# Kernel tuning notes

Measured on AMD Instinct MI355X. Metric: run time of the kernel, lower is better.

Reference implementation:

```python
import jax, jax.numpy as jnp
import numpy as np

KH = KW = 3
STRIDE = 1
ITERATIONS = 2
EPS = 1e-7


def _squash(s):
    # squash along last axis (capsule dim)
    sn = jnp.sum(s * s, axis=-1, keepdims=True)
    return (sn / (1.0 + sn)) * s / jnp.sqrt(sn + EPS)


def setup_inputs() -> dict:
    key = jax.random.key(0)
    k1, k2 = jax.random.split(key)
    x = jax.random.normal(k1, (4, 14, 14, 32, 8), dtype=jnp.float32)
    # W: [1,1,1,filters_out, caps_per_patch=3*3*32, dims_out=16, dims_in=8], stddev=0.1 init
    W = 0.1 * jax.random.normal(k2, (1, 1, 1, 32, 288, 16, 8), dtype=jnp.float32)
    return {"x": x, "W": W}


def reference(x, W):
    B, H, Wd, Fin, Din = x.shape
    Ho = (H - KH) // STRIDE + 1
    Wo = (Wd - KW) // STRIDE + 1
    # Patch extraction, channel order (kh, kw, Fin) to match tf.image.extract_patches
    patches = jnp.stack(
        [x[:, i:i + Ho * STRIDE:STRIDE, j:j + Wo * STRIDE:STRIDE]
         for i in range(KH) for j in range(KW)],
        axis=3,
    )  # [B,Ho,Wo,KH*KW,Fin,Din]
    patches = patches.reshape(B, Ho, Wo, KH * KW * Fin, Din)  # [B,Ho,Wo,C,Di]

    Wm = W[0, 0, 0]  # [F, C, Do, Di]
    F, C, Do, _ = Wm.shape
    # predictions[b,h,w,f,c,o] = sum_i W[f,c,o,i] * patches[b,h,w,c,i]
    preds = jnp.einsum('fcoi,bhwci->bhwfco', Wm, patches)

    logits = jnp.zeros((B, Ho, Wo, F, C), dtype=preds.dtype)
    outputs = jnp.zeros((B, Ho, Wo, F, Do), dtype=preds.dtype)
    for _ in range(ITERATIONS):
        # agreement = predictions^T @ outputs over the dims_out axis
        agreement = jnp.einsum('bhwfco,bhwfo->bhwfc', preds, outputs)
        logits = logits + agreement
        # NOTE: original code softmaxes over axis=3 (the filters_out axis)
        cc = jax.nn.softmax(logits, axis=3)  # [B,Ho,Wo,F,C]
        centroids = jnp.sum(cc[..., None] * preds, axis=4)  # [B,Ho,Wo,F,Do]
        outputs = _squash(centroids)
    return outputs
```

## Files before the change

### kernel.cpp

```cpp
#include <hip/hip_runtime.h>

#define NB   4
#define H_IN 14
#define W_IN 14
#define FIN  32
#define DI   8
#define F    32
#define C    288
#define DO   16
#define HO   12
#define WO   12
#define NPOS (NB*HO*WO)
#define EPS  1e-7f

#define CH   16
#define CC   (C/CH)
#define GP   8
#define GRID (CH*(NPOS/GP))

#define KTOT (C*DI)

#define W2H_BYTES  ((size_t)F*C*DO*DI*2)
#define WH_BYTES   ((size_t)F*C*DO*DI*2)
#define PH_BYTES   ((size_t)NPOS*KTOT*2)
#define PART_BYTES ((size_t)CH*NPOS*F*DO*4)
#define OUT1_BYTES ((size_t)NPOS*F*DO*4)

#define CVT_W2H 576
#define CVT_WH  576
#define CVT_PH  648
#define CVT_GRID (CVT_W2H + CVT_WH + CVT_PH)

typedef _Float16 h2 __attribute__((ext_vector_type(2)));
typedef _Float16 h8v __attribute__((ext_vector_type(8)));
typedef float    f4v __attribute__((ext_vector_type(4)));

__device__ __forceinline__ unsigned int pack2(float a, float b) {
    h2 v; v.x = (_Float16)a; v.y = (_Float16)b;
    return __builtin_bit_cast(unsigned int, v);
}

__device__ __forceinline__ float dot8h(const uint4 w, const uint4 v, float acc) {
#if __has_builtin(__builtin_amdgcn_fdot2)
    acc = __builtin_amdgcn_fdot2(__builtin_bit_cast(h2, w.x), __builtin_bit_cast(h2, v.x), acc, false);
    acc = __builtin_amdgcn_fdot2(__builtin_bit_cast(h2, w.y), __builtin_bit_cast(h2, v.y), acc, false);
    acc = __builtin_amdgcn_fdot2(__builtin_bit_cast(h2, w.z), __builtin_bit_cast(h2, v.z), acc, false);
    acc = __builtin_amdgcn_fdot2(__builtin_bit_cast(h2, w.w), __builtin_bit_cast(h2, v.w), acc, false);
#else
    const h2 w0 = __builtin_bit_cast(h2, w.x), v0 = __builtin_bit_cast(h2, v.x);
    const h2 w1 = __builtin_bit_cast(h2, w.y), v1 = __builtin_bit_cast(h2, v.y);
    const h2 w2 = __builtin_bit_cast(h2, w.z), v2 = __builtin_bit_cast(h2, v.z);
    const h2 w3 = __builtin_bit_cast(h2, w.w), v3 = __builtin_bit_cast(h2, v.w);
    acc += (float)w0.x*(float)v0.x + (float)w0.y*(float)v0.y
         + (float)w1.x*(float)v1.x + (float)w1.y*(float)v1.y
         + (float)w2.x*(float)v2.x + (float)w2.y*(float)v2.y
         + (float)w3.x*(float)v3.x + (float)w3.y*(float)v3.y;
#endif
    return acc;
}

__device__ __forceinline__ int xbase_of(int pos) {
    const int b = pos/(HO*WO), rem = pos%(HO*WO), ho = rem/WO, wo = rem%WO;
    return ((b*H_IN + ho)*W_IN + wo)*FIN*DI;
}

__device__ __forceinline__ int coff_of(int c) {
    const int slab = c >> 5, fin = c & 31;
    const int kh = slab/3, kw = slab%3;
    return (kh*W_IN + kw)*FIN*DI + fin*DI;
}

__global__ __launch_bounds__(256) void kernConv(const float* __restrict__ Wt,
                                                const float* __restrict__ x,
                                                unsigned short* __restrict__ W2h,
                                                unsigned short* __restrict__ Wh,
                                                unsigned short* __restrict__ Ph) {
    const int b = blockIdx.x;
    if (b < CVT_W2H) {
        const int idx = b*256 + threadIdx.x;
        const int f = idx & 31, o = (idx >> 5) & 15, c = idx >> 9;
        const float* src = Wt + ((size_t)(f*C + c)*DO + o)*DI;
        const float4 a = *(const float4*)src;
        const float4 bb = *(const float4*)(src + 4);
        uint4 r;
        r.x = pack2(a.x, a.y);   r.y = pack2(a.z, a.w);
        r.z = pack2(bb.x, bb.y); r.w = pack2(bb.z, bb.w);
        ((uint4*)W2h)[idx] = r;
    } else if (b < CVT_W2H + CVT_WH) {
        const int idx = (b - CVT_W2H)*256 + threadIdx.x;
        const float* src = Wt + (size_t)idx*8;
        const float4 a = *(const float4*)src;
        const float4 bb = *(const float4*)(src + 4);
        uint4 r;
        r.x = pack2(a.x, a.y);   r.y = pack2(a.z, a.w);
        r.z = pack2(bb.x, bb.y); r.w = pack2(bb.z, bb.w);
        ((uint4*)Wh)[idx] = r;
    } else {
        const int pc = (b - CVT_W2H - CVT_WH)*256 + threadIdx.x;
        const int pos = pc / C, c = pc % C;
        const float* src = x + xbase_of(pos) + coff_of(c);
        const float4 a = *(const float4*)src;
        const float4 bb = *(const float4*)(src + 4);
        uint4 r;
        r.x = pack2(a.x, a.y);   r.y = pack2(a.z, a.w);
        r.z = pack2(bb.x, bb.y); r.w = pack2(bb.z, bb.w);
        ((uint4*)Ph)[pc] = r;
    }
}

__global__ __launch_bounds__(256) void kernM1(const unsigned short* __restrict__ Ph,
                                              const unsigned short* __restrict__ Wh,
                                              float* __restrict__ out1)
{
    const int lane = threadIdx.x & 63;
    const int wv   = threadIdx.x >> 6;
    const int f    = blockIdx.x & 31;
    const int pt   = (blockIdx.x >> 5)*4 + wv;
    const int pos0 = pt*16;
    const int n    = lane & 15, q = lane >> 4;

    const unsigned short* pa = Ph + (size_t)(pos0 + n)*KTOT + q*8;
    const unsigned short* pb = Wh + ((size_t)(f*C + q)*DO + n)*DI;

    f4v acc0 = {0.f,0.f,0.f,0.f}, acc1 = {0.f,0.f,0.f,0.f};
    #pragma unroll 4
    for (int s = 0; s < KTOT/32; s += 2) {
        const h8v a0 = *(const h8v*)(pa + (size_t)s*32);
        const h8v b0 = *(const h8v*)(pb + (size_t)s*4*DO*DI);
        const h8v a1 = *(const h8v*)(pa + (size_t)(s+1)*32);
        const h8v b1 = *(const h8v*)(pb + (size_t)(s+1)*4*DO*DI);
        acc0 = __builtin_amdgcn_mfma_f32_16x16x32_f16(a0, b0, acc0, 0, 0, 0);
        acc1 = __builtin_amdgcn_mfma_f32_16x16x32_f16(a1, b1, acc1, 0, 0, 0);
    }

    #pragma unroll
    for (int r = 0; r < 4; ++r) {
        const float v = (acc0[r] + acc1[r]) * (1.f/32.f);
        float sq = v*v;
        sq += __shfl_xor(sq, 1);
        sq += __shfl_xor(sq, 2);
        sq += __shfl_xor(sq, 4);
        sq += __shfl_xor(sq, 8);
        const float sc = (sq/(1.f + sq)) * rsqrtf(sq + EPS);
        out1[(size_t)(pos0 + q*4 + r)*512 + f*DO + n] = v * sc;
    }
}

__global__ __launch_bounds__(256) void kern2n(const unsigned short* __restrict__ Ph,
                                              const unsigned short* __restrict__ W2h,
                                              const float* __restrict__ out1,
                                              float* __restrict__ part2)
{
    __shared__ float red[2][4][GP][32];
    __shared__ float ccs[2][GP][32];

    const int tid = threadIdx.x;
    const int f  = tid & 31;
    const int og = tid >> 5;
    const int o0 = 2*og, o1 = o0 + 1;
    const int wv = tid >> 6;
    const int half = (tid >> 5) & 1;
    const int ch = blockIdx.x & (CH-1);
    const int pg = blockIdx.x >> 4;

    int poff[GP];
    #pragma unroll
    for (int p = 0; p < GP; ++p) poff[p] = (pg*GP + p)*KTOT;

    float u0[GP], u1[GP];
    #pragma unroll
    for (int p = 0; p < GP; ++p) {
        const float* up = out1 + (size_t)(pg*GP + p)*512 + f*DO;
        u0[p] = up[o0];
        u1[p] = up[o1];
    }

    const uint4* W2h4 = (const uint4*)W2h;
    const int c0 = ch*CC;

    float acc0[GP], acc1[GP];
    #pragma unroll
    for (int p = 0; p < GP; ++p) { acc0[p] = 0.f; acc1[p] = 0.f; }

    #pragma unroll 1
    for (int cl = 0; cl < CC; ++cl) {
        const int c = c0 + cl;
        const int buf = cl & 1;
        const uint4 w0 = W2h4[(size_t)(c*DO + o0)*F + f];
        const uint4 w1 = W2h4[(size_t)(c*DO + o1)*F + f];

        float pred0[GP], pred1[GP];
        #pragma unroll
        for (int p = 0; p < GP; ++p) {
            const uint4 xv = *(const uint4*)(Ph + poff[p] + c*DI);
            pred0[p] = dot8h(w0, xv, 0.f);
            pred1[p] = dot8h(w1, xv, 0.f);
        }

        #pragma unroll
        for (int p = 0; p < GP; ++p) {
            float ap = pred0[p]*u0[p] + pred1[p]*u1[p];
            ap += __shfl_xor(ap, 32);
            if (half == 0) red[buf][wv][p][f] = ap;
        }
        __syncthreads();

        {
            const int p2 = tid >> 5, f2 = tid & 31;
            const float agr = red[buf][0][p2][f2] + red[buf][1][p2][f2]
                            + red[buf][2][p2][f2] + red[buf][3][p2][f2];
            float m = agr;
            m = fmaxf(m, __shfl_xor(m, 1));
            m = fmaxf(m, __shfl_xor(m, 2));
            m = fmaxf(m, __shfl_xor(m, 4));
            m = fmaxf(m, __shfl_xor(m, 8));
            m = fmaxf(m, __shfl_xor(m, 16));
            const float e = __expf(agr - m);
            float s = e;
            s += __shfl_xor(s, 1);
            s += __shfl_xor(s, 2);
            s += __shfl_xor(s, 4);
            s += __shfl_xor(s, 8);
            s += __shfl_xor(s, 16);
            ccs[buf][p2][f2] = e / s;
        }
        __syncthreads();

        #pragma unroll
        for (int p = 0; p < GP; ++p) {
            const float cv = ccs[buf][p][f];
            acc0[p] += cv*pred0[p];
            acc1[p] += cv*pred1[p];
        }
    }

    #pragma unroll
    for (int p = 0; p < GP; ++p) {
        const size_t base = ((size_t)(ch*NPOS + pg*GP + p))*DO;
        part2[(base + o0)*F + f] = acc0[p];
        part2[(base + o1)*F + f] = acc1[p];
    }
}

__global__ __launch_bounds__(256) void kern3(const float* __restrict__ part2,
                                             float* __restrict__ out)
{
    const int tid = threadIdx.x;
    const int f = tid & 31, p = tid >> 5;
    const int pos = blockIdx.x*8 + p;

    float cent[DO];
    #pragma unroll
    for (int o = 0; o < DO; ++o) cent[o] = 0.f;
    #pragma unroll 1
    for (int k = 0; k < CH; ++k) {
        const float* s = part2 + (size_t)(k*NPOS + pos)*512 + f;
        #pragma unroll
        for (int o = 0; o < DO; ++o) cent[o] += s[o*F];
    }
    float sn = 0.f;
    #pragma unroll
    for (int o = 0; o < DO; ++o) sn += cent[o]*cent[o];
    const float sc = (sn/(1.f + sn)) * rsqrtf(sn + EPS);
    float* dst = out + ((size_t)pos*F + f)*DO;
    #pragma unroll
    for (int o = 0; o < DO; ++o) dst[o] = cent[o]*sc;
}

__device__ __forceinline__ float dot8(const float4* __restrict__ w,
                                      const float4 p0, const float4 p1) {
    float4 a = w[0], b = w[1];
    return a.x*p0.x + a.y*p0.y + a.z*p0.z + a.w*p0.w
         + b.x*p1.x + b.y*p1.y + b.z*p1.z + b.w*p1.w;
}

__global__ __launch_bounds__(256) void capsule_kernel_f32(
    const float* __restrict__ x, const float* __restrict__ Wt,
    float* __restrict__ out)
{
    __shared__ float patch[C*DI];
    __shared__ float cent[F*DO];
    __shared__ float out1[F*DO];
    __shared__ float agr[F*C];
    __shared__ float scale_s[F];

    const int tid = threadIdx.x;
    const int pos = blockIdx.x;
    const int b   = pos / (HO*WO);
    const int rem = pos % (HO*WO);
    const int ho  = rem / WO;
    const int wo  = rem % WO;

    #pragma unroll
    for (int slab = 0; slab < 9; ++slab) {
        const int kh = slab / 3, kw = slab % 3;
        const float* src = x + (((b*H_IN + ho + kh)*W_IN + (wo + kw))*FIN)*DI;
        patch[slab*256 + tid] = src[tid];
    }
    __syncthreads();

    const float4* pv = (const float4*)patch;

    {
        const int fo0 = tid, fo1 = tid + 256;
        const int f0 = fo0 >> 4, o0 = fo0 & 15;
        const int f1 = fo1 >> 4, o1 = fo1 & 15;
        float acc0 = 0.f, acc1 = 0.f;
        for (int c = 0; c < C; ++c) {
            const float4 p0 = pv[c*2], p1 = pv[c*2+1];
            acc0 += dot8((const float4*)(Wt + ((f0*C + c)*DO + o0)*DI), p0, p1);
            acc1 += dot8((const float4*)(Wt + ((f1*C + c)*DO + o1)*DI), p0, p1);
        }
        cent[fo0] = acc0 * (1.f/32.f);
        cent[fo1] = acc1 * (1.f/32.f);
    }
    __syncthreads();

    if (tid < F) {
        float sn = 0.f;
        #pragma unroll
        for (int o = 0; o < DO; ++o) { float v = cent[tid*DO + o]; sn += v*v; }
        const float sc = (sn/(1.f + sn)) * rsqrtf(sn + EPS);
        #pragma unroll
        for (int o = 0; o < DO; ++o) out1[tid*DO + o] = cent[tid*DO + o] * sc;
    }
    __syncthreads();

    #pragma unroll 1
    for (int r = 0; r < (F*C)/256; ++r) {
        const int pp = tid + 256*r;
        const int f = pp / C, c = pp % C;
        const float4* wrow = (const float4*)(Wt + (f*C + c)*DO*DI);
        const float4 p0 = pv[c*2], p1 = pv[c*2+1];
        float a = 0.f;
        #pragma unroll
        for (int o = 0; o < DO; ++o) a += dot8(wrow + o*2, p0, p1) * out1[f*DO + o];
        agr[pp] = a;
    }
    __syncthreads();

    for (int c = tid; c < C; c += 256) {
        float m = -1e30f;
        #pragma unroll
        for (int f = 0; f < F; ++f) m = fmaxf(m, agr[f*C + c]);
        float s = 0.f;
        #pragma unroll
        for (int f = 0; f < F; ++f) {
            const float e = __expf(agr[f*C + c] - m);
            agr[f*C + c] = e; s += e;
        }
        const float inv = 1.f / s;
        #pragma unroll
        for (int f = 0; f < F; ++f) agr[f*C + c] *= inv;
    }
    __syncthreads();

    {
        const int fo0 = tid, fo1 = tid + 256;
        const int f0 = fo0 >> 4, o0 = fo0 & 15;
        const int f1 = fo1 >> 4, o1 = fo1 & 15;
        float acc0 = 0.f, acc1 = 0.f;
        for (int c = 0; c < C; ++c) {
            const float4 p0 = pv[c*2], p1 = pv[c*2+1];
            acc0 += agr[f0*C + c] * dot8((const float4*)(Wt + ((f0*C + c)*DO + o0)*DI), p0, p1);
            acc1 += agr[f1*C + c] * dot8((const float4*)(Wt + ((f1*C + c)*DO + o1)*DI), p0, p1);
        }
        cent[fo0] = acc0;
        cent[fo1] = acc1;
    }
    __syncthreads();

    if (tid < F) {
        float sn = 0.f;
        #pragma unroll
        for (int o = 0; o < DO; ++o) { float v = cent[tid*DO + o]; sn += v*v; }
        scale_s[tid] = (sn/(1.f + sn)) * rsqrtf(sn + EPS);
    }
    __syncthreads();

    out[pos*(F*DO) + tid]       = cent[tid]       * scale_s[tid >> 4];
    out[pos*(F*DO) + tid + 256] = cent[tid + 256] * scale_s[(tid >> 4) + 16];
}

extern "C" void kernel_launch(void* const* d_in, const int* in_sizes, int n_in,
                              void* d_out, int out_size, void* d_ws, size_t ws_size,
                              hipStream_t stream) {
    const float* x  = (const float*)d_in[0];
    const float* Wt = (const float*)d_in[1];
    float* out = (float*)d_out;

    if (ws_size >= W2H_BYTES + WH_BYTES + PH_BYTES + PART_BYTES + OUT1_BYTES) {
        char* p = (char*)d_ws;
        unsigned short* W2h = (unsigned short*)p;            p += W2H_BYTES;
        unsigned short* Wh  = (unsigned short*)p;            p += WH_BYTES;
        unsigned short* Ph  = (unsigned short*)p;            p += PH_BYTES;
        float* part = (float*)p;                             p += PART_BYTES;
        float* out1 = (float*)p;

        kernConv<<<CVT_GRID, 256, 0, stream>>>(Wt, x, W2h, Wh, Ph);
        kernM1<<<(F/1)*9, 256, 0, stream>>>(Ph, Wh, out1);
        kern2n<<<GRID, 256, 0, stream>>>(Ph, W2h, out1, part);
        kern3<<<NPOS/8, 256, 0, stream>>>(part, out);
    } else {
        capsule_kernel_f32<<<NPOS, 256, 0, stream>>>(x, Wt, out);
    }
}
```

Measured before the change: 138.1 us.

## Stage patch tile in LDS shared across waves in kernM1; coalesce W2h reads

kernM1 now loads each 16-position patch tile once into padded shared memory. The four waves of a block each compute a different output filter from that shared tile, instead of each wave streaming the patches from global memory for its own position tile. The W2h conversion now reads the weights linearly and scatters its writes into the same [c][o][f] layout as before, swapping strided reads for strided writes. The shared tile uses about 74KB of LDS per block, which may limit occupancy and adds a block-wide barrier before the MFMA loop.

```diff
diff --git a/kernel.cpp b/kernel.cpp
--- a/kernel.cpp
+++ b/kernel.cpp
@@ -19,6 +19,7 @@
 #define GRID (CH*(NPOS/GP))
 
 #define KTOT (C*DI)
+#define KPAD 2312
 
 #define W2H_BYTES  ((size_t)F*C*DO*DI*2)
 #define WH_BYTES   ((size_t)F*C*DO*DI*2)
@@ -78,14 +79,16 @@
     const int b = blockIdx.x;
     if (b < CVT_W2H) {
         const int idx = b*256 + threadIdx.x;
-        const int f = idx & 31, o = (idx >> 5) & 15, c = idx >> 9;
-        const float* src = Wt + ((size_t)(f*C + c)*DO + o)*DI;
+        const float* src = Wt + (size_t)idx*8;
         const float4 a = *(const float4*)src;
         const float4 bb = *(const float4*)(src + 4);
         uint4 r;
         r.x = pack2(a.x, a.y);   r.y = pack2(a.z, a.w);
         r.z = pack2(bb.x, bb.y); r.w = pack2(bb.z, bb.w);
-        ((uint4*)W2h)[idx] = r;
+        const int o = idx & 15;
+        const int c = (idx >> 4) % C;
+        const int f = idx / (C*DO);
+        ((uint4*)W2h)[(size_t)(c*DO + o)*F + f] = r;
     } else if (b < CVT_W2H + CVT_WH) {
         const int idx = (b - CVT_W2H)*256 + threadIdx.x;
         const float* src = Wt + (size_t)idx*8;
@@ -112,22 +115,35 @@
                                               const unsigned short* __restrict__ Wh,
                                               float* __restrict__ out1)
 {
-    const int lane = threadIdx.x & 63;
-    const int wv   = threadIdx.x >> 6;
-    const int f    = blockIdx.x & 31;
-    const int pt   = (blockIdx.x >> 5)*4 + wv;
+    __shared__ unsigned short As[16][KPAD];
+
+    const int tid  = threadIdx.x;
+    const int lane = tid & 63;
+    const int wv   = tid >> 6;
+    const int pt   = blockIdx.x >> 3;
+    const int fg   = blockIdx.x & 7;
+    const int f    = wv*8 + fg;
     const int pos0 = pt*16;
     const int n    = lane & 15, q = lane >> 4;
 
-    const unsigned short* pa = Ph + (size_t)(pos0 + n)*KTOT + q*8;
+    #pragma unroll
+    for (int r = 0; r < 18; ++r) {
+        const int linear = r*256 + tid;
+        const int row = linear / 288, col8 = linear % 288;
+        const uint4 v = *(const uint4*)(Ph + (size_t)(pos0 + row)*KTOT + col8*8);
+        *(uint4*)&As[row][col8*8] = v;
+    }
+    __syncthreads();
+
+    const unsigned short* pa = &As[n][q*8];
     const unsigned short* pb = Wh + ((size_t)(f*C + q)*DO + n)*DI;
 
     f4v acc0 = {0.f,0.f,0.f,0.f}, acc1 = {0.f,0.f,0.f,0.f};
     #pragma unroll 4
     for (int s = 0; s < KTOT/32; s += 2) {
-        const h8v a0 = *(const h8v*)(pa + (size_t)s*32);
+        const h8v a0 = *(const h8v*)(pa + s*32);
         const h8v b0 = *(const h8v*)(pb + (size_t)s*4*DO*DI);
-        const h8v a1 = *(const h8v*)(pa + (size_t)(s+1)*32);
+        const h8v a1 = *(const h8v*)(pa + (s+1)*32);
         const h8v b1 = *(const h8v*)(pb + (size_t)(s+1)*4*DO*DI);
         acc0 = __builtin_amdgcn_mfma_f32_16x16x32_f16(a0, b0, acc0, 0, 0, 0);
         acc1 = __builtin_amdgcn_mfma_f32_16x16x32_f16(a1, b1, acc1, 0, 0, 0);
@@ -398,7 +414,7 @@
         float* out1 = (float*)p;
 
         kernConv<<<CVT_GRID, 256, 0, stream>>>(Wt, x, W2h, Wh, Ph);
-        kernM1<<<(F/1)*9, 256, 0, stream>>>(Ph, Wh, out1);
+        kernM1<<<36*8, 256, 0, stream>>>(Ph, Wh, out1);
         kern2n<<<GRID, 256, 0, stream>>>(Ph, W2h, out1, part);
         kern3<<<NPOS/8, 256, 0, stream>>>(part, out);
     } else {
```

After: 133.5 us, median of 2. 1.03x faster.
